# Kernel tuning notes

Hardware: AMD Instinct MI355X
Metric: run time of the kernel (lower is better)

## Reference

```python
import jax, jax.numpy as jnp
import numpy as np

NEG_INF = -1e30


def setup_inputs() -> dict:
    key = jax.random.key(0)
    k1, k2, k3, k4, k5, k6 = jax.random.split(key, 6)
    T, B = 256, 8
    Din, Dm, A = 256, 256, 128
    input = jax.random.normal(k1, (T, B, Din), dtype=jnp.float32)
    memory = jax.random.normal(k2, (T, B, Dm), dtype=jnp.float32)
    memory_mask = jax.random.randint(k3, (T, B), 0, 2, dtype=jnp.int32)
    # first Linear weight [A, Din+Dm] split into input / memory halves (additive decomposition)
    scale1 = 1.0 / np.sqrt(Din + Dm)
    Wi = jax.random.uniform(k4, (Din, A), minval=-scale1, maxval=scale1, dtype=jnp.float32)
    Wm = jax.random.uniform(k5, (Dm, A), minval=-scale1, maxval=scale1, dtype=jnp.float32)
    # second Linear weight [1, A] -> vector [A]
    scale2 = 1.0 / np.sqrt(A)
    v = jax.random.uniform(k6, (A,), minval=-scale2, maxval=scale2, dtype=jnp.float32)
    return {"input": input, "memory": memory, "memory_mask": memory_mask,
            "Wi": Wi, "Wm": Wm, "v": v}


def reference(input, memory, memory_mask, Wi, Wm, v):
    # input: [T, B, Din], memory: [T, B, Dm], memory_mask: [T, B]
    # Additive (Bahdanau) scores: v . tanh(Wi x_s + Wm m_t). Concat+Linear on
    # [x; m] with block weight [Wi; Wm] equals the sum of the two projections.
    ip = jnp.einsum('tbd,da->tba', input, Wi)[:, None]    # [T, 1, B, A]
    mp = jnp.einsum('tbd,da->tba', memory, Wm)[None]      # [1, T, B, A]
    logits = jnp.einsum('stba,a->stb', jnp.tanh(ip + mp), v)  # [T, T, B]
    masked = jnp.where(memory_mask[None] != 0, logits, NEG_INF)
    score = jax.nn.softmax(masked, axis=1)                # softmax over key dim
    # NOTE: original module weights `input` (not memory) as values.
    context = jnp.einsum('stb,tbd->sbd', score, input)    # [T, B, Din]
    return jnp.concatenate([context, input], axis=-1)      # [T, B, 2*Din]
```

## Files before the change

### kernel.cpp

```cpp
#include <hip/hip_runtime.h>

#define T_DIM 256
#define B_DIM 8
#define DIN   256
#define DM    256
#define A_DIM 128
#define NEG_INF_F (-1e30f)
#define PRESCALE 2.885390081777927f
#define PROJ_TT 4
#define CTX_ST  4

__global__ __launch_bounds__(256) void proj_kernel(
    const float* __restrict__ input, const float* __restrict__ memory,
    const float* __restrict__ Wi, const float* __restrict__ Wm,
    float* __restrict__ EIP, float* __restrict__ EM)
{
    __shared__ float xin[PROJ_TT][DIN];
    __shared__ float xmem[PROJ_TT][DM];
    const int row0 = blockIdx.x * PROJ_TT;
    const int tid  = threadIdx.x;

    #pragma unroll
    for (int r = 0; r < PROJ_TT; ++r) {
        xin[r][tid]  = input[(row0 + r) * DIN + tid];
        xmem[r][tid] = memory[(row0 + r) * DM + tid];
    }
    __syncthreads();

    if (tid < A_DIM) {
        const int a = tid;
        float acc[PROJ_TT] = {0.f, 0.f, 0.f, 0.f};
        #pragma unroll 8
        for (int d = 0; d < DIN; ++d) {
            const float w = Wi[d * A_DIM + a];
            #pragma unroll
            for (int r = 0; r < PROJ_TT; ++r)
                acc[r] = fmaf(xin[r][d], w, acc[r]);
        }
        #pragma unroll
        for (int r = 0; r < PROJ_TT; ++r)
            EIP[(row0 + r) * A_DIM + a] =
                __builtin_amdgcn_exp2f(acc[r] * PRESCALE);
    } else {
        const int a = tid - A_DIM;
        float acc[PROJ_TT] = {0.f, 0.f, 0.f, 0.f};
        #pragma unroll 8
        for (int d = 0; d < DM; ++d) {
            const float w = Wm[d * A_DIM + a];
            #pragma unroll
            for (int r = 0; r < PROJ_TT; ++r)
                acc[r] = fmaf(xmem[r][d], w, acc[r]);
        }
        #pragma unroll
        for (int r = 0; r < PROJ_TT; ++r) {
            const int t = (row0 + r) / B_DIM, b = (row0 + r) % B_DIM;
            EM[(b * A_DIM + a) * T_DIM + t] =
                __builtin_amdgcn_exp2f(acc[r] * PRESCALE);
        }
    }
}

__device__ inline float warp_red_max(float v) {
    #pragma unroll
    for (int o = 32; o > 0; o >>= 1) v = fmaxf(v, __shfl_xor(v, o, 64));
    return v;
}
__device__ inline float warp_red_sum(float v) {
    #pragma unroll
    for (int o = 32; o > 0; o >>= 1) v += __shfl_xor(v, o, 64);
    return v;
}

__global__ __launch_bounds__(256) void logits_kernel(
    const int* __restrict__ mask, const float* __restrict__ v,
    const float* __restrict__ EIP, const float* __restrict__ EM,
    float* __restrict__ SC)
{
    __shared__ float eip_s[A_DIM];
    __shared__ float vs[A_DIM];
    __shared__ float red[4];

    const int blk = blockIdx.x;
    const int b   = blk % B_DIM;
    const int s   = blk / B_DIM;
    const int tid = threadIdx.x;
    const int lane = tid & 63;
    const int wave = tid >> 6;

    if (tid < A_DIM) {
        vs[tid]    = v[tid];
        eip_s[tid] = EIP[(s * B_DIM + b) * A_DIM + tid];
    }
    __syncthreads();

    const int t = tid;
    float acc = 0.f;
    const float* em_base = EM + (size_t)(b * A_DIM) * T_DIM + t;
    #pragma unroll 8
    for (int a = 0; a < A_DIM; ++a) {
        const float em = em_base[(size_t)a * T_DIM];
        const float e  = eip_s[a] * em;
        acc = fmaf(vs[a], __builtin_amdgcn_rcpf(e + 1.f), acc);
    }

    const bool valid = (mask[t * B_DIM + b] != 0);
    const float l = valid ? (-2.f * acc) : NEG_INF_F;

    float m = warp_red_max(l);
    if (lane == 0) red[wave] = m;
    __syncthreads();
    m = fmaxf(fmaxf(red[0], red[1]), fmaxf(red[2], red[3]));
    const float e = __expf(l - m);
    float su = warp_red_sum(e);
    __syncthreads();
    if (lane == 0) red[wave] = su;
    __syncthreads();
    su = (red[0] + red[1]) + (red[2] + red[3]);
    SC[(s * B_DIM + b) * T_DIM + t] = e * __builtin_amdgcn_rcpf(su);
}

__global__ __launch_bounds__(256) void context_kernel(
    const float* __restrict__ input, const float* __restrict__ SC,
    float* __restrict__ out)
{
    __shared__ float sc_s[CTX_ST][T_DIM];
    const int blk = blockIdx.x;
    const int b   = blk % B_DIM;
    const int s0  = (blk / B_DIM) * CTX_ST;
    const int tid = threadIdx.x;

    for (int i = tid; i < CTX_ST * T_DIM; i += 256) {
        const int r = i >> 8, t = i & (T_DIM - 1);
        sc_s[r][t] = SC[((s0 + r) * B_DIM + b) * T_DIM + t];
    }
    __syncthreads();

    const int d = tid;
    float c[CTX_ST] = {0.f, 0.f, 0.f, 0.f};
    const float* in_b = input + b * DIN + d;
    #pragma unroll 8
    for (int t2 = 0; t2 < T_DIM; ++t2) {
        const float xv = in_b[(size_t)t2 * B_DIM * DIN];
        #pragma unroll
        for (int r = 0; r < CTX_ST; ++r)
            c[r] = fmaf(sc_s[r][t2], xv, c[r]);
    }

    #pragma unroll
    for (int r = 0; r < CTX_ST; ++r) {
        const int row = (s0 + r) * B_DIM + b;
        out[(size_t)row * (2 * DIN) + d]       = c[r];
        out[(size_t)row * (2 * DIN) + DIN + d] = input[row * DIN + d];
    }
}

extern "C" void kernel_launch(void* const* d_in, const int* in_sizes, int n_in,
                              void* d_out, int out_size, void* d_ws, size_t ws_size,
                              hipStream_t stream) {
    const float* input  = (const float*)d_in[0];
    const float* memory = (const float*)d_in[1];
    const int*   mask   = (const int*)d_in[2];
    const float* Wi     = (const float*)d_in[3];
    const float* Wm     = (const float*)d_in[4];
    const float* v      = (const float*)d_in[5];
    float* out = (float*)d_out;

    float* EIP = (float*)d_ws;
    float* EM  = EIP + (size_t)T_DIM * B_DIM * A_DIM;
    float* SC  = EM  + (size_t)B_DIM * A_DIM * T_DIM;

    proj_kernel<<<(T_DIM * B_DIM) / PROJ_TT, 256, 0, stream>>>(input, memory, Wi, Wm, EIP, EM);
    logits_kernel<<<T_DIM * B_DIM, 256, 0, stream>>>(mask, v, EIP, EM, SC);
    context_kernel<<<(T_DIM / CTX_ST) * B_DIM, 256, 0, stream>>>(input, SC, out);
}
```

Measured before the change: 106.4 us.

## Fuse logits softmax and context into one kernel with two query rows per block

Merges the logits/softmax kernel and the context kernel into one kernel in which each block handles two query rows for one batch. The softmax scores stay in shared memory instead of going through a global scratch buffer, one launch is dropped, and each EM value loaded serves two query rows. In exchange, the context stage now reuses each input load across only two rows instead of four, which doubles the input re-reads there.

```diff
diff --git a/kernel.cpp b/kernel.cpp
--- a/kernel.cpp
+++ b/kernel.cpp
@@ -8,7 +8,7 @@
 #define NEG_INF_F (-1e30f)
 #define PRESCALE 2.885390081777927f
 #define PROJ_TT 4
-#define CTX_ST  4
+#define S_PAIR  2
 
 __global__ __launch_bounds__(256) void proj_kernel(
     const float* __restrict__ input, const float* __restrict__ memory,
@@ -71,86 +71,81 @@
     return v;
 }
 
-__global__ __launch_bounds__(256) void logits_kernel(
-    const int* __restrict__ mask, const float* __restrict__ v,
-    const float* __restrict__ EIP, const float* __restrict__ EM,
-    float* __restrict__ SC)
+__global__ __launch_bounds__(256) void attn_kernel(
+    const float* __restrict__ input, const int* __restrict__ mask,
+    const float* __restrict__ v, const float* __restrict__ EIP,
+    const float* __restrict__ EM, float* __restrict__ out)
 {
-    __shared__ float eip_s[A_DIM];
+    __shared__ float eip_s[S_PAIR][A_DIM];
     __shared__ float vs[A_DIM];
-    __shared__ float red[4];
+    __shared__ float sc[S_PAIR][T_DIM];
+    __shared__ float redm[S_PAIR][4];
 
     const int blk = blockIdx.x;
     const int b   = blk % B_DIM;
-    const int s   = blk / B_DIM;
+    const int s0  = (blk / B_DIM) * S_PAIR;
     const int tid = threadIdx.x;
     const int lane = tid & 63;
     const int wave = tid >> 6;
 
     if (tid < A_DIM) {
-        vs[tid]    = v[tid];
-        eip_s[tid] = EIP[(s * B_DIM + b) * A_DIM + tid];
+        vs[tid]          = v[tid];
+        eip_s[0][tid]    = EIP[((s0 + 0) * B_DIM + b) * A_DIM + tid];
+        eip_s[1][tid]    = EIP[((s0 + 1) * B_DIM + b) * A_DIM + tid];
     }
     __syncthreads();
 
     const int t = tid;
-    float acc = 0.f;
+    float acc0 = 0.f, acc1 = 0.f;
     const float* em_base = EM + (size_t)(b * A_DIM) * T_DIM + t;
     #pragma unroll 8
     for (int a = 0; a < A_DIM; ++a) {
         const float em = em_base[(size_t)a * T_DIM];
-        const float e  = eip_s[a] * em;
-        acc = fmaf(vs[a], __builtin_amdgcn_rcpf(e + 1.f), acc);
+        const float va = vs[a];
+        const float e0 = eip_s[0][a] * em;
+        const float e1 = eip_s[1][a] * em;
+        acc0 = fmaf(va, __builtin_amdgcn_rcpf(e0 + 1.f), acc0);
+        acc1 = fmaf(va, __builtin_amdgcn_rcpf(e1 + 1.f), acc1);
     }
 
     const bool valid = (mask[t * B_DIM + b] != 0);
-    const float l = valid ? (-2.f * acc) : NEG_INF_F;
+    const float l0 = valid ? (-2.f * acc0) : NEG_INF_F;
+    const float l1 = valid ? (-2.f * acc1) : NEG_INF_F;
 
-    float m = warp_red_max(l);
-    if (lane == 0) red[wave] = m;
+    float m0 = warp_red_max(l0), m1 = warp_red_max(l1);
+    if (lane == 0) { redm[0][wave] = m0; redm[1][wave] = m1; }
     __syncthreads();
-    m = fmaxf(fmaxf(red[0], red[1]), fmaxf(red[2], red[3]));
-    const float e = __expf(l - m);
-    float su = warp_red_sum(e);
+    m0 = fmaxf(fmaxf(redm[0][0], redm[0][1]), fmaxf(redm[0][2], redm[0][3]));
+    m1 = fmaxf(fmaxf(redm[1][0], redm[1][1]), fmaxf(redm[1][2], redm[1][3]));
+    const float e0 = __expf(l0 - m0);
+    const float e1 = __expf(l1 - m1);
+    float su0 = warp_red_sum(e0), su1 = warp_red_sum(e1);
     __syncthreads();
-    if (lane == 0) red[wave] = su;
+    if (lane == 0) { redm[0][wave] = su0; redm[1][wave] = su1; }
     __syncthreads();
-    su = (red[0] + red[1]) + (red[2] + red[3]);
-    SC[(s * B_DIM + b) * T_DIM + t] = e * __builtin_amdgcn_rcpf(su);
-}
-
-__global__ __launch_bounds__(256) void context_kernel(
-    const float* __restrict__ input, const float* __restrict__ SC,
-    float* __restrict__ out)
-{
-    __shared__ float sc_s[CTX_ST][T_DIM];
-    const int blk = blockIdx.x;
-    const int b   = blk % B_DIM;
-    const int s0  = (blk / B_DIM) * CTX_ST;
-    const int tid = threadIdx.x;
-
-    for (int i = tid; i < CTX_ST * T_DIM; i += 256) {
-        const int r = i >> 8, t = i & (T_DIM - 1);
-        sc_s[r][t] = SC[((s0 + r) * B_DIM + b) * T_DIM + t];
-    }
+    su0 = (redm[0][0] + redm[0][1]) + (redm[0][2] + redm[0][3]);
+    su1 = (redm[1][0] + redm[1][1]) + (redm[1][2] + redm[1][3]);
+    sc[0][t] = e0 * __builtin_amdgcn_rcpf(su0);
+    sc[1][t] = e1 * __builtin_amdgcn_rcpf(su1);
     __syncthreads();
 
     const int d = tid;
-    float c[CTX_ST] = {0.f, 0.f, 0.f, 0.f};
+    float c0 = 0.f, c1 = 0.f;
     const float* in_b = input + b * DIN + d;
     #pragma unroll 8
     for (int t2 = 0; t2 < T_DIM; ++t2) {
         const float xv = in_b[(size_t)t2 * B_DIM * DIN];
-        #pragma unroll
-        for (int r = 0; r < CTX_ST; ++r)
-            c[r] = fmaf(sc_s[r][t2], xv, c[r]);
+        c0 = fmaf(sc[0][t2], xv, c0);
+        c1 = fmaf(sc[1][t2], xv, c1);
     }
 
-    #pragma unroll
-    for (int r = 0; r < CTX_ST; ++r) {
-        const int row = (s0 + r) * B_DIM + b;
-        out[(size_t)row * (2 * DIN) + d]       = c[r];
-        out[(size_t)row * (2 * DIN) + DIN + d] = input[row * DIN + d];
+    {
+        const int r0 = (s0 + 0) * B_DIM + b;
+        const int r1 = (s0 + 1) * B_DIM + b;
+        out[(size_t)r0 * (2 * DIN) + d]       = c0;
+        out[(size_t)r0 * (2 * DIN) + DIN + d] = input[r0 * DIN + d];
+        out[(size_t)r1 * (2 * DIN) + d]       = c1;
+        out[(size_t)r1 * (2 * DIN) + DIN + d] = input[r1 * DIN + d];
     }
 }
 
@@ -167,9 +162,7 @@
 
     float* EIP = (float*)d_ws;
     float* EM  = EIP + (size_t)T_DIM * B_DIM * A_DIM;
-    float* SC  = EM  + (size_t)B_DIM * A_DIM * T_DIM;
 
     proj_kernel<<<(T_DIM * B_DIM) / PROJ_TT, 256, 0, stream>>>(input, memory, Wi, Wm, EIP, EM);
-    logits_kernel<<<T_DIM * B_DIM, 256, 0, stream>>>(mask, v, EIP, EM, SC);
-    context_kernel<<<(T_DIM / CTX_ST) * B_DIM, 256, 0, stream>>>(input, SC, out);
+    attn_kernel<<<(T_DIM / S_PAIR) * B_DIM, 256, 0, stream>>>(input, mask, v, EIP, EM, out);
 }
```

After: 101.5 us. 4.6% less time.
